# Optimization experiments

Hardware: AMD Instinct MI355X
Metric: run time of the kernel (lower is better)

The kernel has to match this reference:

```python
import jax, jax.numpy as jnp
import numpy as np

TOP_K = 2  # matches init kwarg top_k


def setup_inputs() -> dict:
    key = jax.random.key(0)
    k1, k2, k3 = jax.random.split(key, 3)
    N, D, H, E = 8192, 2048, 2048, 8
    x = jax.random.normal(k1, (N, D), dtype=jnp.float32)
    Wg = jax.random.normal(k2, (D, E), dtype=jnp.float32) * (1.0 / np.sqrt(D))
    bg = jnp.zeros((E,), dtype=jnp.float32)
    We = jax.random.normal(k3, (E, D, H), dtype=jnp.float32) * (1.0 / np.sqrt(D))
    be = jnp.zeros((E, H), dtype=jnp.float32)
    return {"x": x, "Wg": Wg, "bg": bg, "We": We, "be": be}


def reference(x, Wg, bg, We, be):
    # Gating: softmax over experts, then keep only top-k weights per token.
    gate = jax.nn.softmax(x @ Wg + bg, axis=-1)          # [N, E]
    top_v, top_i = jax.lax.top_k(gate, TOP_K)            # [N, K]
    E = gate.shape[-1]
    # Sparse combine weights: zeros except top-k entries (weights NOT renormalized,
    # matching the original which uses raw softmax scores).
    comb = jnp.sum(jax.nn.one_hot(top_i, E, dtype=gate.dtype) * top_v[..., None], axis=1)  # [N, E]
    # Per-expert linear applied to every token (dense dispatch), then weighted sum.
    expert_out = jnp.einsum('nd,edh->neh', x, We) + be   # [N, E, H]
    out = jnp.einsum('ne,neh->nh', comb, expert_out)     # [N, H]
    return out
```

## Files before the change

### kernel.cpp

```cpp
#include <hip/hip_runtime.h>

#define N_TOK 8192
#define DIM   2048
#define HID   2048
#define NE    8

typedef unsigned short u16;
typedef __attribute__((ext_vector_type(4))) float f4v;
typedef __attribute__((ext_vector_type(8))) short s8v;
typedef __attribute__((ext_vector_type(4))) unsigned short us4;
typedef __attribute__((ext_vector_type(4))) unsigned int u32x4;

__device__ __forceinline__ u16 f2bf(float f) {
  union { float f; unsigned int u; } c; c.f = f;
  unsigned int u = c.u;
  unsigned int r = (u + 0x7FFFu + ((u >> 16) & 1u)) >> 16;
  return (u16)r;
}

__device__ __forceinline__ void gll16(const void* g, void* l) {
  __builtin_amdgcn_global_load_lds(
      (const __attribute__((address_space(1))) void*)g,
      (__attribute__((address_space(3))) void*)l, 16, 0, 0);
}

__global__ __launch_bounds__(256) void gating_kernel(
    const float* __restrict__ x, const float* __restrict__ Wg,
    const float* __restrict__ bg, int* __restrict__ sel,
    float* __restrict__ wslot, u16* __restrict__ xb)
{
  __shared__ float wg_lds[NE][DIM];
  #pragma unroll
  for (int i = 0; i < 16; ++i) {
    int f = threadIdx.x + 256 * i;
    int d = f >> 1, ep = (f & 1) * 4;
    float4 w = reinterpret_cast<const float4*>(Wg)[f];
    wg_lds[ep + 0][d] = w.x; wg_lds[ep + 1][d] = w.y;
    wg_lds[ep + 2][d] = w.z; wg_lds[ep + 3][d] = w.w;
  }
  __syncthreads();

  int wave = threadIdx.x >> 6, lane = threadIdx.x & 63;
  #pragma unroll 2
  for (int j = 0; j < 4; ++j) {
    int n = blockIdx.x * 16 + wave * 4 + j;
    const float4* x4 = reinterpret_cast<const float4*>(x + (size_t)n * DIM);
    float acc[NE] = {0.f,0.f,0.f,0.f,0.f,0.f,0.f,0.f};
    #pragma unroll
    for (int i = 0; i < 8; ++i) {
      int d4 = lane + 64 * i;
      float4 xv = x4[d4];
      if (xb) {
        us4 u = {f2bf(xv.x), f2bf(xv.y), f2bf(xv.z), f2bf(xv.w)};
        *reinterpret_cast<us4*>(xb + (size_t)n * DIM + d4 * 4) = u;
      }
      #pragma unroll
      for (int e = 0; e < NE; ++e) {
        float4 w = *reinterpret_cast<const float4*>(&wg_lds[e][d4 * 4]);
        acc[e] += xv.x * w.x + xv.y * w.y + xv.z * w.z + xv.w * w.w;
      }
    }
    #pragma unroll
    for (int e = 0; e < NE; ++e)
      #pragma unroll
      for (int off = 32; off; off >>= 1)
        acc[e] += __shfl_xor(acc[e], off);

    if (lane == 0) {
      float m = -1e30f;
      #pragma unroll
      for (int e = 0; e < NE; ++e) { acc[e] += bg[e]; m = fmaxf(m, acc[e]); }
      float p[NE]; float s = 0.f;
      #pragma unroll
      for (int e = 0; e < NE; ++e) { p[e] = expf(acc[e] - m); s += p[e]; }
      float inv = 1.0f / s;
      int e1 = 0; float v1 = p[0];
      #pragma unroll
      for (int e = 1; e < NE; ++e) if (p[e] > v1) { v1 = p[e]; e1 = e; }
      int e2 = -1; float v2 = -1.f;
      #pragma unroll
      for (int e = 0; e < NE; ++e) if (e != e1 && p[e] > v2) { v2 = p[e]; e2 = e; }
      sel[n] = e1 | (e2 << 4);
      wslot[n] = v1 * inv;
      wslot[N_TOK + n] = v2 * inv;
    }
  }
}

__global__ __launch_bounds__(256) void build_lists_kernel(
    const int* __restrict__ sel, int* __restrict__ counts, int* __restrict__ lists)
{
  __shared__ int wsum[4];
  __shared__ int runbase;
  int b = blockIdx.x;
  int s = b >> 3, e = b & 7;
  int t = threadIdx.x, lane = t & 63, wave = t >> 6;
  if (t == 0) runbase = 0;
  __syncthreads();
  int* listp = lists + (size_t)b * N_TOK;
  for (int base = 0; base < N_TOK; base += 256) {
    int n = base + t;
    int sv = sel[n];
    int field = s ? (sv >> 4) : (sv & 15);
    bool p = (field == e);
    unsigned long long mask = __ballot(p);
    int rank = __popcll(mask & ((1ull << lane) - 1ull));
    int wtot = __popcll(mask);
    if (lane == 0) wsum[wave] = wtot;
    __syncthreads();
    int wbase = 0;
    #pragma unroll
    for (int w = 0; w < 4; ++w) wbase += (w < wave) ? wsum[w] : 0;
    int tot = wsum[0] + wsum[1] + wsum[2] + wsum[3];
    if (p) listp[runbase + wbase + rank] = n;
    __syncthreads();
    if (t == 0) runbase += tot;
    __syncthreads();
  }
  if (t == 0) counts[b] = runbase;
}

__global__ __launch_bounds__(256) void transpose_we_kernel(const float* __restrict__ We,
                                                           u16* __restrict__ WeT)
{
  __shared__ u16 tile[64][72];
  int e = blockIdx.z;
  int k0 = blockIdx.y * 64;
  int h0 = blockIdx.x * 64;
  const float* src = We + (size_t)e * DIM * HID + (size_t)k0 * HID + h0;
  #pragma unroll
  for (int i = 0; i < 4; ++i) {
    int flat = threadIdx.x + 256 * i;
    int kk = flat >> 4, c4 = flat & 15;
    float4 v = *reinterpret_cast<const float4*>(src + (size_t)kk * HID + c4 * 4);
    us4 u = {f2bf(v.x), f2bf(v.y), f2bf(v.z), f2bf(v.w)};
    *reinterpret_cast<us4*>(&tile[kk][c4 * 4]) = u;
  }
  __syncthreads();
  u16* dst = WeT + (size_t)e * HID * DIM + (size_t)h0 * DIM + k0;
  #pragma unroll
  for (int i = 0; i < 4; ++i) {
    int flat = threadIdx.x + 256 * i;
    int hh = flat >> 4, c4 = flat & 15;
    us4 u = {tile[c4 * 4 + 0][hh], tile[c4 * 4 + 1][hh],
             tile[c4 * 4 + 2][hh], tile[c4 * 4 + 3][hh]};
    *reinterpret_cast<us4*>(dst + (size_t)hh * DIM + c4 * 4) = u;
  }
}

__device__ __forceinline__ void mma_step(const u16* A_lds, const u16* B_lds,
                                         int lane, int wm, int wn, f4v acc[4][4])
{
  int lrow = lane & 15, lkg = lane >> 4;
  #pragma unroll
  for (int kk2 = 0; kk2 < 2; ++kk2) {
    s8v a[4], b[4];
    unsigned int koff = (unsigned int)(kk2 * 64 + lkg * 16);
    #pragma unroll
    for (int i = 0; i < 4; ++i) {
      unsigned int arow = (unsigned int)(wm + i * 16 + lrow);
      a[i] = *reinterpret_cast<const s8v*>(
          reinterpret_cast<const char*>(A_lds) + ((arow * 128u + koff) ^ ((arow & 7u) << 4)));
      unsigned int brow = (unsigned int)(wn + i * 16 + lrow);
      b[i] = *reinterpret_cast<const s8v*>(
          reinterpret_cast<const char*>(B_lds) + ((brow * 128u + koff) ^ ((brow & 7u) << 4)));
    }
    #pragma unroll
    for (int mi = 0; mi < 4; ++mi)
      #pragma unroll
      for (int ni = 0; ni < 4; ++ni)
        acc[mi][ni] = __builtin_amdgcn_mfma_f32_16x16x32_bf16(a[mi], b[ni], acc[mi][ni], 0, 0, 0);
  }
}

template <int PHASE, bool BF16SRC>
__global__ __launch_bounds__(256) void moe_gemm(
    const void* __restrict__ Asrc, const void* __restrict__ Bsrc,
    const float* __restrict__ be, const int* __restrict__ counts,
    const int* __restrict__ lists, const float* __restrict__ wslot,
    float* __restrict__ out)
{
  __shared__ __align__(16) u16 A_lds[128 * 64];
  __shared__ __align__(16) u16 B_lds[128 * 64];
  __shared__ int   tok_lds[128];
  __shared__ float wgt_lds[128];

  const int ntile = blockIdx.x;
  const int e  = blockIdx.y >> 6;
  const int mt = blockIdx.y & 63;
  const int cnt = counts[PHASE * NE + e];
  if (mt * 128 >= cnt) return;

  const int t = threadIdx.x;
  if (t < 128) {
    int r = mt * 128 + t;
    int rc = (r < cnt) ? r : (cnt - 1);
    int tok = lists[(PHASE * NE + e) * N_TOK + rc];
    tok_lds[t] = tok;
    wgt_lds[t] = wslot[PHASE * N_TOK + tok];
  }
  __syncthreads();

  const int lane = t & 63, wid = t >> 6;
  const int wm = (wid & 1) * 64, wn = (wid >> 1) * 64;

  f4v acc[4][4];
  f4v zero = {0.f, 0.f, 0.f, 0.f};
  #pragma unroll
  for (int mi = 0; mi < 4; ++mi)
    #pragma unroll
    for (int ni = 0; ni < 4; ++ni) acc[mi][ni] = zero;

  if constexpr (!BF16SRC) {
    const float* xf  = reinterpret_cast<const float*>(Asrc);
    const float* wef = reinterpret_cast<const float*>(Bsrc) + (size_t)e * DIM * HID;
    const float* ap[8]; unsigned int ab[8];
    #pragma unroll
    for (int i = 0; i < 8; ++i) {
      int flat = t + 256 * i;
      int row = flat >> 4, c4 = flat & 15;
      ap[i] = xf + (size_t)tok_lds[row] * DIM + c4 * 4;
      ab[i] = ((unsigned int)(row * 128 + c4 * 8)) ^ (((unsigned int)row & 7u) << 4);
    }
    int bn = t & 127, bh = t >> 7;
    const float* bp0 = wef + (size_t)(bh * 32) * HID + ntile * 128 + bn;
    unsigned int nswz = (((unsigned int)bn & 7u) << 4);
    for (int kt = 0; kt < DIM / 64; ++kt) {
      #pragma unroll
      for (int i = 0; i < 8; ++i) {
        float4 v = *reinterpret_cast<const float4*>(ap[i] + kt * 64);
        us4 u = {f2bf(v.x), f2bf(v.y), f2bf(v.z), f2bf(v.w)};
        *reinterpret_cast<us4*>(reinterpret_cast<char*>(A_lds) + ab[i]) = u;
      }
      const float* bp = bp0 + (size_t)(kt * 64) * HID;
      #pragma unroll
      for (int kb = 0; kb < 8; ++kb) {
        float f0 = bp[(kb * 4 + 0) * HID];
        float f1 = bp[(kb * 4 + 1) * HID];
        float f2 = bp[(kb * 4 + 2) * HID];
        float f3 = bp[(kb * 4 + 3) * HID];
        us4 u = {f2bf(f0), f2bf(f1), f2bf(f2), f2bf(f3)};
        unsigned int byte = ((unsigned int)(bn * 128 + bh * 64 + kb * 8)) ^ nswz;
        *reinterpret_cast<us4*>(reinterpret_cast<char*>(B_lds) + byte) = u;
      }
      __syncthreads();
      mma_step(A_lds, B_lds, lane, wm, wn, acc);
      __syncthreads();
    }
  } else {
    const u16* xbp = reinterpret_cast<const u16*>(Asrc);
    const u16* web = reinterpret_cast<const u16*>(Bsrc) + (size_t)e * DIM * HID;
    const int r8 = lane >> 3;
    const unsigned int ssw = ((unsigned int)((lane & 7) ^ r8)) << 4;
    const char* srcA[4]; const char* srcB[4];
    #pragma unroll
    for (int i = 0; i < 4; ++i) {
      int row = wid * 32 + i * 8 + r8;
      srcA[i] = reinterpret_cast<const char*>(xbp + (size_t)tok_lds[row] * DIM) + ssw;
      srcB[i] = reinterpret_cast<const char*>(web + (size_t)(ntile * 128 + row) * DIM) + ssw;
    }
    for (int kt = 0; kt < DIM / 64; ++kt) {
      #pragma unroll
      for (int i = 0; i < 4; ++i) {
        gll16(srcA[i] + kt * 128, reinterpret_cast<char*>(A_lds) + wid * 4096 + i * 1024);
        gll16(srcB[i] + kt * 128, reinterpret_cast<char*>(B_lds) + wid * 4096 + i * 1024);
      }
      __syncthreads();
      mma_step(A_lds, B_lds, lane, wm, wn, acc);
      __syncthreads();
    }
  }

  const float* bev = be + (size_t)e * HID + ntile * 128;
  #pragma unroll
  for (int ni = 0; ni < 4; ++ni) {
    int col = wn + ni * 16 + (lane & 15);
    float bevv = bev[col];
    #pragma unroll
    for (int mi = 0; mi < 4; ++mi) {
      #pragma unroll
      for (int q = 0; q < 4; ++q) {
        int row = wm + mi * 16 + (lane >> 4) * 4 + q;
        if (mt * 128 + row < cnt) {
          int tok = tok_lds[row];
          float w = wgt_lds[row];
          float v = w * (acc[mi][ni][q] + bevv);
          float* o = out + (size_t)tok * HID + ntile * 128 + col;
          if (PHASE == 0) *o = v; else *o += v;
        }
      }
    }
  }
}

extern "C" void kernel_launch(void* const* d_in, const int* in_sizes, int n_in,
                              void* d_out, int out_size, void* d_ws, size_t ws_size,
                              hipStream_t stream) {
  const float* x  = (const float*)d_in[0];
  const float* Wg = (const float*)d_in[1];
  const float* bg = (const float*)d_in[2];
  const float* We = (const float*)d_in[3];
  const float* be = (const float*)d_in[4];
  float* out = (float*)d_out;
  char* ws = (char*)d_ws;

  int*   counts = (int*)ws;
  int*   sel    = (int*)(ws + 256);
  float* wslot  = (float*)(ws + 256 + sizeof(int) * N_TOK);
  int*   lists  = (int*)(ws + 256 + sizeof(int) * N_TOK + sizeof(float) * 2 * N_TOK);
  size_t small_end = 256 + sizeof(int) * N_TOK + sizeof(float) * 2 * N_TOK
                   + sizeof(int) * 2 * NE * N_TOK;
  size_t off_x = (small_end + 255) & ~(size_t)255;
  size_t xbytes = (size_t)N_TOK * DIM * 2;
  size_t off_w = off_x + xbytes;
  size_t wbytes = (size_t)NE * DIM * HID * 2;
  bool full = (ws_size >= off_w + wbytes);

  u16* xb = full ? (u16*)(ws + off_x) : nullptr;

  hipLaunchKernelGGL(gating_kernel, dim3(512), dim3(256), 0, stream,
                     x, Wg, bg, sel, wslot, xb);
  hipLaunchKernelGGL(build_lists_kernel, dim3(16), dim3(256), 0, stream,
                     sel, counts, lists);

  dim3 ggrid(HID / 128, NE * (N_TOK / 128));
  if (full) {
    u16* wt = (u16*)(ws + off_w);
    hipLaunchKernelGGL(transpose_we_kernel, dim3(HID / 64, DIM / 64, NE), dim3(256), 0, stream, We, wt);
    hipLaunchKernelGGL((moe_gemm<0, true>), ggrid, dim3(256), 0, stream,
                       (const void*)xb, (const void*)wt, be, counts, lists, wslot, out);
    hipLaunchKernelGGL((moe_gemm<1, true>), ggrid, dim3(256), 0, stream,
                       (const void*)xb, (const void*)wt, be, counts, lists, wslot, out);
  } else {
    hipLaunchKernelGGL((moe_gemm<0, false>), ggrid, dim3(256), 0, stream,
                       (const void*)x, (const void*)We, be, counts, lists, wslot, out);
    hipLaunchKernelGGL((moe_gemm<1, false>), ggrid, dim3(256), 0, stream,
                       (const void*)x, (const void*)We, be, counts, lists, wslot, out);
  }
}
```

Baseline: 450.2 us.

## Compact GEMM grid with tile descriptors and chunk expert weight conversion by workspace size

A new single-thread kernel builds a compact list of (expert, row-tile) descriptors, so the grouped GEMM launches only about 71 row-tile slots instead of 512 mostly-idle blocks that exit early. The expert weight transpose/convert is also split into chunks sized to the available workspace. This allows the bf16 global_load_lds path to be used for weights even with a small workspace, at the cost of re-converting chunks between phases. With a full workspace (c=8) this runs as one transpose plus two GEMMs, so the main intended saving is fewer launched empty blocks. The serial descriptor kernel adds a small extra launch.

```diff
diff --git a/kernel.cpp b/kernel.cpp
--- a/kernel.cpp
+++ b/kernel.cpp
@@ -120,6 +120,22 @@
   if (t == 0) counts[b] = runbase;
 }
 
+__global__ void build_desc_kernel(const int* __restrict__ counts,
+                                  int* __restrict__ gfirst, int* __restrict__ desc)
+{
+  if (threadIdx.x == 0 && blockIdx.x == 0) {
+    for (int s = 0; s < 2; ++s) {
+      int tc = 0;
+      for (int e = 0; e < NE; ++e) {
+        gfirst[s * 9 + e] = tc;
+        int nt = (counts[s * NE + e] + 127) >> 7;
+        for (int i = 0; i < nt; ++i) desc[s * 71 + tc++] = (e << 8) | i;
+      }
+      gfirst[s * 9 + 8] = tc;
+    }
+  }
+}
+
 __global__ __launch_bounds__(256) void transpose_we_kernel(const float* __restrict__ We,
                                                            u16* __restrict__ WeT)
 {
@@ -173,12 +189,39 @@
   }
 }
 
-template <int PHASE, bool BF16SRC>
+__device__ __forceinline__ void gemm_epilogue(
+    const f4v acc[4][4], const float* be, const int* tok_lds, const float* wgt_lds,
+    int e, int ntile, int mt, int cnt, int lane, int wm, int wn, float* out, int phase)
+{
+  const float* bev = be + (size_t)e * HID + ntile * 128;
+  #pragma unroll
+  for (int ni = 0; ni < 4; ++ni) {
+    int col = wn + ni * 16 + (lane & 15);
+    float bevv = bev[col];
+    #pragma unroll
+    for (int mi = 0; mi < 4; ++mi) {
+      #pragma unroll
+      for (int q = 0; q < 4; ++q) {
+        int row = wm + mi * 16 + (lane >> 4) * 4 + q;
+        if (mt * 128 + row < cnt) {
+          int tok = tok_lds[row];
+          float w = wgt_lds[row];
+          float v = w * (acc[mi][ni][q] + bevv);
+          float* o = out + (size_t)tok * HID + ntile * 128 + col;
+          if (phase == 0) *o = v; else *o += v;
+        }
+      }
+    }
+  }
+}
+
+template <int PHASE, bool ABF16>
 __global__ __launch_bounds__(256) void moe_gemm(
-    const void* __restrict__ Asrc, const void* __restrict__ Bsrc,
+    const void* __restrict__ Asrc, const u16* __restrict__ wt,
     const float* __restrict__ be, const int* __restrict__ counts,
+    const int* __restrict__ gfirst, const int* __restrict__ desc,
     const int* __restrict__ lists, const float* __restrict__ wslot,
-    float* __restrict__ out)
+    float* __restrict__ out, int ce, int cnume)
 {
   __shared__ __align__(16) u16 A_lds[128 * 64];
   __shared__ __align__(16) u16 B_lds[128 * 64];
@@ -186,10 +229,14 @@
   __shared__ float wgt_lds[128];
 
   const int ntile = blockIdx.x;
-  const int e  = blockIdx.y >> 6;
-  const int mt = blockIdx.y & 63;
+  const int base = gfirst[PHASE * 9 + ce];
+  const int end  = gfirst[PHASE * 9 + ce + cnume];
+  const int idx  = base + (int)blockIdx.y;
+  if (idx >= end) return;
+  const int d  = desc[PHASE * 71 + idx];
+  const int e  = d >> 8;
+  const int mt = d & 255;
   const int cnt = counts[PHASE * NE + e];
-  if (mt * 128 >= cnt) return;
 
   const int t = threadIdx.x;
   if (t < 128) {
@@ -211,9 +258,36 @@
     #pragma unroll
     for (int ni = 0; ni < 4; ++ni) acc[mi][ni] = zero;
 
-  if constexpr (!BF16SRC) {
-    const float* xf  = reinterpret_cast<const float*>(Asrc);
-    const float* wef = reinterpret_cast<const float*>(Bsrc) + (size_t)e * DIM * HID;
+  const u16* web = wt + (size_t)(e - ce) * DIM * HID;
+  const int r8 = lane >> 3;
+  const unsigned int ssw = ((unsigned int)((lane & 7) ^ r8)) << 4;
+  const char* srcB[4];
+  #pragma unroll
+  for (int i = 0; i < 4; ++i) {
+    int row = wid * 32 + i * 8 + r8;
+    srcB[i] = reinterpret_cast<const char*>(web + (size_t)(ntile * 128 + row) * DIM) + ssw;
+  }
+
+  if constexpr (ABF16) {
+    const u16* xbp = reinterpret_cast<const u16*>(Asrc);
+    const char* srcA[4];
+    #pragma unroll
+    for (int i = 0; i < 4; ++i) {
+      int row = wid * 32 + i * 8 + r8;
+      srcA[i] = reinterpret_cast<const char*>(xbp + (size_t)tok_lds[row] * DIM) + ssw;
+    }
+    for (int kt = 0; kt < DIM / 64; ++kt) {
+      #pragma unroll
+      for (int i = 0; i < 4; ++i) {
+        gll16(srcA[i] + kt * 128, reinterpret_cast<char*>(A_lds) + wid * 4096 + i * 1024);
+        gll16(srcB[i] + kt * 128, reinterpret_cast<char*>(B_lds) + wid * 4096 + i * 1024);
+      }
+      __syncthreads();
+      mma_step(A_lds, B_lds, lane, wm, wn, acc);
+      __syncthreads();
+    }
+  } else {
+    const float* xf = reinterpret_cast<const float*>(Asrc);
     const float* ap[8]; unsigned int ab[8];
     #pragma unroll
     for (int i = 0; i < 8; ++i) {
@@ -222,75 +296,102 @@
       ap[i] = xf + (size_t)tok_lds[row] * DIM + c4 * 4;
       ab[i] = ((unsigned int)(row * 128 + c4 * 8)) ^ (((unsigned int)row & 7u) << 4);
     }
-    int bn = t & 127, bh = t >> 7;
-    const float* bp0 = wef + (size_t)(bh * 32) * HID + ntile * 128 + bn;
-    unsigned int nswz = (((unsigned int)bn & 7u) << 4);
     for (int kt = 0; kt < DIM / 64; ++kt) {
+      #pragma unroll
+      for (int i = 0; i < 4; ++i)
+        gll16(srcB[i] + kt * 128, reinterpret_cast<char*>(B_lds) + wid * 4096 + i * 1024);
       #pragma unroll
       for (int i = 0; i < 8; ++i) {
         float4 v = *reinterpret_cast<const float4*>(ap[i] + kt * 64);
         us4 u = {f2bf(v.x), f2bf(v.y), f2bf(v.z), f2bf(v.w)};
         *reinterpret_cast<us4*>(reinterpret_cast<char*>(A_lds) + ab[i]) = u;
       }
-      const float* bp = bp0 + (size_t)(kt * 64) * HID;
-      #pragma unroll
-      for (int kb = 0; kb < 8; ++kb) {
-        float f0 = bp[(kb * 4 + 0) * HID];
-        float f1 = bp[(kb * 4 + 1) * HID];
-        float f2 = bp[(kb * 4 + 2) * HID];
-        float f3 = bp[(kb * 4 + 3) * HID];
-        us4 u = {f2bf(f0), f2bf(f1), f2bf(f2), f2bf(f3)};
-        unsigned int byte = ((unsigned int)(bn * 128 + bh * 64 + kb * 8)) ^ nswz;
-        *reinterpret_cast<us4*>(reinterpret_cast<char*>(B_lds) + byte) = u;
-      }
       __syncthreads();
       mma_step(A_lds, B_lds, lane, wm, wn, acc);
       __syncthreads();
     }
-  } else {
-    const u16* xbp = reinterpret_cast<const u16*>(Asrc);
-    const u16* web = reinterpret_cast<const u16*>(Bsrc) + (size_t)e * DIM * HID;
-    const int r8 = lane >> 3;
-    const unsigned int ssw = ((unsigned int)((lane & 7) ^ r8)) << 4;
-    const char* srcA[4]; const char* srcB[4];
-    #pragma unroll
-    for (int i = 0; i < 4; ++i) {
-      int row = wid * 32 + i * 8 + r8;
-      srcA[i] = reinterpret_cast<const char*>(xbp + (size_t)tok_lds[row] * DIM) + ssw;
-      srcB[i] = reinterpret_cast<const char*>(web + (size_t)(ntile * 128 + row) * DIM) + ssw;
-    }
-    for (int kt = 0; kt < DIM / 64; ++kt) {
-      #pragma unroll
-      for (int i = 0; i < 4; ++i) {
-        gll16(srcA[i] + kt * 128, reinterpret_cast<char*>(A_lds) + wid * 4096 + i * 1024);
-        gll16(srcB[i] + kt * 128, reinterpret_cast<char*>(B_lds) + wid * 4096 + i * 1024);
-      }
-      __syncthreads();
-      mma_step(A_lds, B_lds, lane, wm, wn, acc);
-      __syncthreads();
-    }
-  }
-
-  const float* bev = be + (size_t)e * HID + ntile * 128;
-  #pragma unroll
-  for (int ni = 0; ni < 4; ++ni) {
-    int col = wn + ni * 16 + (lane & 15);
-    float bevv = bev[col];
-    #pragma unroll
-    for (int mi = 0; mi < 4; ++mi) {
-      #pragma unroll
-      for (int q = 0; q < 4; ++q) {
-        int row = wm + mi * 16 + (lane >> 4) * 4 + q;
-        if (mt * 128 + row < cnt) {
-          int tok = tok_lds[row];
-          float w = wgt_lds[row];
-          float v = w * (acc[mi][ni][q] + bevv);
-          float* o = out + (size_t)tok * HID + ntile * 128 + col;
-          if (PHASE == 0) *o = v; else *o += v;
-        }
-      }
-    }
-  }
+  }
+
+  gemm_epilogue(acc, be, tok_lds, wgt_lds, e, ntile, mt, cnt, lane, wm, wn, out, PHASE);
+}
+
+template <int PHASE>
+__global__ __launch_bounds__(256) void moe_gemm_f32b(
+    const float* __restrict__ xf, const float* __restrict__ Wef,
+    const float* __restrict__ be, const int* __restrict__ counts,
+    const int* __restrict__ gfirst, const int* __restrict__ desc,
+    const int* __restrict__ lists, const float* __restrict__ wslot,
+    float* __restrict__ out)
+{
+  __shared__ __align__(16) u16 A_lds[128 * 64];
+  __shared__ __align__(16) u16 B_lds[128 * 64];
+  __shared__ int   tok_lds[128];
+  __shared__ float wgt_lds[128];
+
+  const int ntile = blockIdx.x;
+  const int idx = gfirst[PHASE * 9 + 0] + (int)blockIdx.y;
+  if (idx >= gfirst[PHASE * 9 + 8]) return;
+  const int d  = desc[PHASE * 71 + idx];
+  const int e  = d >> 8;
+  const int mt = d & 255;
+  const int cnt = counts[PHASE * NE + e];
+
+  const int t = threadIdx.x;
+  if (t < 128) {
+    int r = mt * 128 + t;
+    int rc = (r < cnt) ? r : (cnt - 1);
+    int tok = lists[(PHASE * NE + e) * N_TOK + rc];
+    tok_lds[t] = tok;
+    wgt_lds[t] = wslot[PHASE * N_TOK + tok];
+  }
+  __syncthreads();
+
+  const int lane = t & 63, wid = t >> 6;
+  const int wm = (wid & 1) * 64, wn = (wid >> 1) * 64;
+
+  f4v acc[4][4];
+  f4v zero = {0.f, 0.f, 0.f, 0.f};
+  #pragma unroll
+  for (int mi = 0; mi < 4; ++mi)
+    #pragma unroll
+    for (int ni = 0; ni < 4; ++ni) acc[mi][ni] = zero;
+
+  const float* wef = Wef + (size_t)e * DIM * HID;
+  const float* ap[8]; unsigned int ab[8];
+  #pragma unroll
+  for (int i = 0; i < 8; ++i) {
+    int flat = t + 256 * i;
+    int row = flat >> 4, c4 = flat & 15;
+    ap[i] = xf + (size_t)tok_lds[row] * DIM + c4 * 4;
+    ab[i] = ((unsigned int)(row * 128 + c4 * 8)) ^ (((unsigned int)row & 7u) << 4);
+  }
+  int bn = t & 127, bh = t >> 7;
+  const float* bp0 = wef + (size_t)(bh * 32) * HID + ntile * 128 + bn;
+  unsigned int nswz = (((unsigned int)bn & 7u) << 4);
+  for (int kt = 0; kt < DIM / 64; ++kt) {
+    #pragma unroll
+    for (int i = 0; i < 8; ++i) {
+      float4 v = *reinterpret_cast<const float4*>(ap[i] + kt * 64);
+      us4 u = {f2bf(v.x), f2bf(v.y), f2bf(v.z), f2bf(v.w)};
+      *reinterpret_cast<us4*>(reinterpret_cast<char*>(A_lds) + ab[i]) = u;
+    }
+    const float* bp = bp0 + (size_t)(kt * 64) * HID;
+    #pragma unroll
+    for (int kb = 0; kb < 8; ++kb) {
+      float f0 = bp[(kb * 4 + 0) * HID];
+      float f1 = bp[(kb * 4 + 1) * HID];
+      float f2 = bp[(kb * 4 + 2) * HID];
+      float f3 = bp[(kb * 4 + 3) * HID];
+      us4 u = {f2bf(f0), f2bf(f1), f2bf(f2), f2bf(f3)};
+      unsigned int byte = ((unsigned int)(bn * 128 + bh * 64 + kb * 8)) ^ nswz;
+      *reinterpret_cast<us4*>(reinterpret_cast<char*>(B_lds) + byte) = u;
+    }
+    __syncthreads();
+    mma_step(A_lds, B_lds, lane, wm, wn, acc);
+    __syncthreads();
+  }
+
+  gemm_epilogue(acc, be, tok_lds, wgt_lds, e, ntile, mt, cnt, lane, wm, wn, out, PHASE);
 }
 
 extern "C" void kernel_launch(void* const* d_in, const int* in_sizes, int n_in,
@@ -305,36 +406,55 @@
   char* ws = (char*)d_ws;
 
   int*   counts = (int*)ws;
-  int*   sel    = (int*)(ws + 256);
-  float* wslot  = (float*)(ws + 256 + sizeof(int) * N_TOK);
-  int*   lists  = (int*)(ws + 256 + sizeof(int) * N_TOK + sizeof(float) * 2 * N_TOK);
-  size_t small_end = 256 + sizeof(int) * N_TOK + sizeof(float) * 2 * N_TOK
-                   + sizeof(int) * 2 * NE * N_TOK;
-  size_t off_x = (small_end + 255) & ~(size_t)255;
-  size_t xbytes = (size_t)N_TOK * DIM * 2;
-  size_t off_w = off_x + xbytes;
-  size_t wbytes = (size_t)NE * DIM * HID * 2;
-  bool full = (ws_size >= off_w + wbytes);
-
-  u16* xb = full ? (u16*)(ws + off_x) : nullptr;
+  int*   gfirst = (int*)(ws + 64);
+  int*   desc   = (int*)(ws + 256);
+  int*   sel    = (int*)(ws + 1024);
+  float* wslot  = (float*)(ws + 33792);
+  int*   lists  = (int*)(ws + 99328);
+  const size_t base_end = 623616;
+  const size_t xbsz = (size_t)N_TOK * DIM * 2;
+  const size_t pe   = (size_t)DIM * HID * 2;
+
+  int c = 0; bool use_xb = false;
+  const int cands[4] = {8, 4, 2, 1};
+  for (int i = 0; i < 4; ++i) {
+    int cc = cands[i];
+    if (base_end + xbsz + (size_t)cc * pe <= ws_size) { c = cc; use_xb = true; break; }
+    if (base_end + (size_t)cc * pe <= ws_size)        { c = cc; use_xb = false; break; }
+  }
+  u16* xb = use_xb ? (u16*)(ws + base_end) : nullptr;
+  u16* wt = (c > 0) ? (u16*)(ws + base_end + (use_xb ? xbsz : 0)) : nullptr;
 
   hipLaunchKernelGGL(gating_kernel, dim3(512), dim3(256), 0, stream,
                      x, Wg, bg, sel, wslot, xb);
   hipLaunchKernelGGL(build_lists_kernel, dim3(16), dim3(256), 0, stream,
                      sel, counts, lists);
-
-  dim3 ggrid(HID / 128, NE * (N_TOK / 128));
-  if (full) {
-    u16* wt = (u16*)(ws + off_w);
-    hipLaunchKernelGGL(transpose_we_kernel, dim3(HID / 64, DIM / 64, NE), dim3(256), 0, stream, We, wt);
-    hipLaunchKernelGGL((moe_gemm<0, true>), ggrid, dim3(256), 0, stream,
-                       (const void*)xb, (const void*)wt, be, counts, lists, wslot, out);
-    hipLaunchKernelGGL((moe_gemm<1, true>), ggrid, dim3(256), 0, stream,
-                       (const void*)xb, (const void*)wt, be, counts, lists, wslot, out);
+  hipLaunchKernelGGL(build_desc_kernel, dim3(1), dim3(64), 0, stream,
+                     counts, gfirst, desc);
+
+  if (c > 0) {
+    const int nc = NE / c;
+    dim3 tgrid(HID / 64, DIM / 64, c);
+    dim3 ggrid(HID / 128, 63 + c);
+    #define LAUNCH_T(ch) hipLaunchKernelGGL(transpose_we_kernel, tgrid, dim3(256), 0, stream, \
+                           We + (size_t)(ch) * c * DIM * HID, wt)
+    #define LAUNCH_G(PH, ch) do { \
+        if (use_xb) hipLaunchKernelGGL((moe_gemm<PH, true>), ggrid, dim3(256), 0, stream, \
+            (const void*)xb, wt, be, counts, gfirst, desc, lists, wslot, out, (ch) * c, c); \
+        else        hipLaunchKernelGGL((moe_gemm<PH, false>), ggrid, dim3(256), 0, stream, \
+            (const void*)x,  wt, be, counts, gfirst, desc, lists, wslot, out, (ch) * c, c); \
+      } while (0)
+
+    for (int i = 0; i < nc; ++i) { LAUNCH_T(i); LAUNCH_G(0, i); }
+    LAUNCH_G(1, nc - 1);
+    for (int i = nc - 2; i >= 0; --i) { LAUNCH_T(i); LAUNCH_G(1, i); }
+    #undef LAUNCH_T
+    #undef LAUNCH_G
   } else {
-    hipLaunchKernelGGL((moe_gemm<0, false>), ggrid, dim3(256), 0, stream,
-                       (const void*)x, (const void*)We, be, counts, lists, wslot, out);
-    hipLaunchKernelGGL((moe_gemm<1, false>), ggrid, dim3(256), 0, stream,
-                       (const void*)x, (const void*)We, be, counts, lists, wslot, out);
-  }
-}
+    dim3 ggrid(HID / 128, 71);
+    hipLaunchKernelGGL((moe_gemm_f32b<0>), ggrid, dim3(256), 0, stream,
+                       x, We, be, counts, gfirst, desc, lists, wslot, out);
+    hipLaunchKernelGGL((moe_gemm_f32b<1>), ggrid, dim3(256), 0, stream,
+                       x, We, be, counts, gfirst, desc, lists, wslot, out);
+  }
+}
```

New measurement: 451.6 us. About the same (+0.3%).

## Drop bf16 pre-conversion, fuse fp32 conversion into GEMM with register prefetch and compact tile grid

Applied to the files above, without the earlier changes.

Removes the separate We transpose/convert kernel and the bf16 copy of x. The MoE GEMM now reads fp32 inputs directly and converts them to bf16 in registers. The next K-tile is prefetched into registers while the current one runs on MFMA. A descriptor kernel builds a compact list of non-empty (expert, m-tile) pairs, launched over a swizzled 1D grid so blocks no longer exit early. In exchange, the strided scalar fp32 loads of We for the B operand stay uncoalesced and are repeated for every m-tile, and register pressure rises from the 32+ prefetch registers.

```diff
diff --git a/kernel.cpp b/kernel.cpp
--- a/kernel.cpp
+++ b/kernel.cpp
@@ -4,12 +4,12 @@
 #define DIM   2048
 #define HID   2048
 #define NE    8
+#define NKT   (DIM / 64)
 
 typedef unsigned short u16;
 typedef __attribute__((ext_vector_type(4))) float f4v;
 typedef __attribute__((ext_vector_type(8))) short s8v;
 typedef __attribute__((ext_vector_type(4))) unsigned short us4;
-typedef __attribute__((ext_vector_type(4))) unsigned int u32x4;
 
 __device__ __forceinline__ u16 f2bf(float f) {
   union { float f; unsigned int u; } c; c.f = f;
@@ -18,16 +18,10 @@
   return (u16)r;
 }
 
-__device__ __forceinline__ void gll16(const void* g, void* l) {
-  __builtin_amdgcn_global_load_lds(
-      (const __attribute__((address_space(1))) void*)g,
-      (__attribute__((address_space(3))) void*)l, 16, 0, 0);
-}
-
 __global__ __launch_bounds__(256) void gating_kernel(
     const float* __restrict__ x, const float* __restrict__ Wg,
     const float* __restrict__ bg, int* __restrict__ sel,
-    float* __restrict__ wslot, u16* __restrict__ xb)
+    float* __restrict__ wslot)
 {
   __shared__ float wg_lds[NE][DIM];
   #pragma unroll
@@ -50,10 +44,6 @@
     for (int i = 0; i < 8; ++i) {
       int d4 = lane + 64 * i;
       float4 xv = x4[d4];
-      if (xb) {
-        us4 u = {f2bf(xv.x), f2bf(xv.y), f2bf(xv.z), f2bf(xv.w)};
-        *reinterpret_cast<us4*>(xb + (size_t)n * DIM + d4 * 4) = u;
-      }
       #pragma unroll
       for (int e = 0; e < NE; ++e) {
         float4 w = *reinterpret_cast<const float4*>(&wg_lds[e][d4 * 4]);
@@ -120,31 +110,19 @@
   if (t == 0) counts[b] = runbase;
 }
 
-__global__ __launch_bounds__(256) void transpose_we_kernel(const float* __restrict__ We,
-                                                           u16* __restrict__ WeT)
-{
-  __shared__ u16 tile[64][72];
-  int e = blockIdx.z;
-  int k0 = blockIdx.y * 64;
-  int h0 = blockIdx.x * 64;
-  const float* src = We + (size_t)e * DIM * HID + (size_t)k0 * HID + h0;
-  #pragma unroll
-  for (int i = 0; i < 4; ++i) {
-    int flat = threadIdx.x + 256 * i;
-    int kk = flat >> 4, c4 = flat & 15;
-    float4 v = *reinterpret_cast<const float4*>(src + (size_t)kk * HID + c4 * 4);
-    us4 u = {f2bf(v.x), f2bf(v.y), f2bf(v.z), f2bf(v.w)};
-    *reinterpret_cast<us4*>(&tile[kk][c4 * 4]) = u;
-  }
-  __syncthreads();
-  u16* dst = WeT + (size_t)e * HID * DIM + (size_t)h0 * DIM + k0;
-  #pragma unroll
-  for (int i = 0; i < 4; ++i) {
-    int flat = threadIdx.x + 256 * i;
-    int hh = flat >> 4, c4 = flat & 15;
-    us4 u = {tile[c4 * 4 + 0][hh], tile[c4 * 4 + 1][hh],
-             tile[c4 * 4 + 2][hh], tile[c4 * 4 + 3][hh]};
-    *reinterpret_cast<us4*>(dst + (size_t)hh * DIM + c4 * 4) = u;
+__global__ void build_desc_kernel(const int* __restrict__ counts,
+                                  int* __restrict__ gfirst, int* __restrict__ desc)
+{
+  if (threadIdx.x == 0 && blockIdx.x == 0) {
+    for (int s = 0; s < 2; ++s) {
+      int tc = 0;
+      for (int e = 0; e < NE; ++e) {
+        gfirst[s * 9 + e] = tc;
+        int nt = (counts[s * NE + e] + 127) >> 7;
+        for (int i = 0; i < nt; ++i) desc[s * 71 + tc++] = (e << 8) | i;
+      }
+      gfirst[s * 9 + 8] = tc;
+    }
   }
 }
 
@@ -173,10 +151,11 @@
   }
 }
 
-template <int PHASE, bool BF16SRC>
-__global__ __launch_bounds__(256) void moe_gemm(
-    const void* __restrict__ Asrc, const void* __restrict__ Bsrc,
+template <int PHASE>
+__global__ __launch_bounds__(256) void moe_gemm_f32(
+    const float* __restrict__ xf, const float* __restrict__ Wef,
     const float* __restrict__ be, const int* __restrict__ counts,
+    const int* __restrict__ gfirst, const int* __restrict__ desc,
     const int* __restrict__ lists, const float* __restrict__ wslot,
     float* __restrict__ out)
 {
@@ -185,11 +164,15 @@
   __shared__ int   tok_lds[128];
   __shared__ float wgt_lds[128];
 
-  const int ntile = blockIdx.x;
-  const int e  = blockIdx.y >> 6;
-  const int mt = blockIdx.y & 63;
+  const int lin = blockIdx.x;
+  const int swz = (lin & 7) * 142 + (lin >> 3);
+  const int ntile = swz / 71;
+  const int idx   = swz % 71;
+  if (idx >= gfirst[PHASE * 9 + 8]) return;
+  const int d  = desc[PHASE * 71 + idx];
+  const int e  = d >> 8;
+  const int mt = d & 255;
   const int cnt = counts[PHASE * NE + e];
-  if (mt * 128 >= cnt) return;
 
   const int t = threadIdx.x;
   if (t < 128) {
@@ -211,65 +194,62 @@
     #pragma unroll
     for (int ni = 0; ni < 4; ++ni) acc[mi][ni] = zero;
 
-  if constexpr (!BF16SRC) {
-    const float* xf  = reinterpret_cast<const float*>(Asrc);
-    const float* wef = reinterpret_cast<const float*>(Bsrc) + (size_t)e * DIM * HID;
-    const float* ap[8]; unsigned int ab[8];
-    #pragma unroll
-    for (int i = 0; i < 8; ++i) {
-      int flat = t + 256 * i;
-      int row = flat >> 4, c4 = flat & 15;
-      ap[i] = xf + (size_t)tok_lds[row] * DIM + c4 * 4;
-      ab[i] = ((unsigned int)(row * 128 + c4 * 8)) ^ (((unsigned int)row & 7u) << 4);
-    }
-    int bn = t & 127, bh = t >> 7;
-    const float* bp0 = wef + (size_t)(bh * 32) * HID + ntile * 128 + bn;
-    unsigned int nswz = (((unsigned int)bn & 7u) << 4);
-    for (int kt = 0; kt < DIM / 64; ++kt) {
-      #pragma unroll
-      for (int i = 0; i < 8; ++i) {
-        float4 v = *reinterpret_cast<const float4*>(ap[i] + kt * 64);
-        us4 u = {f2bf(v.x), f2bf(v.y), f2bf(v.z), f2bf(v.w)};
-        *reinterpret_cast<us4*>(reinterpret_cast<char*>(A_lds) + ab[i]) = u;
-      }
-      const float* bp = bp0 + (size_t)(kt * 64) * HID;
-      #pragma unroll
-      for (int kb = 0; kb < 8; ++kb) {
-        float f0 = bp[(kb * 4 + 0) * HID];
-        float f1 = bp[(kb * 4 + 1) * HID];
-        float f2 = bp[(kb * 4 + 2) * HID];
-        float f3 = bp[(kb * 4 + 3) * HID];
-        us4 u = {f2bf(f0), f2bf(f1), f2bf(f2), f2bf(f3)};
-        unsigned int byte = ((unsigned int)(bn * 128 + bh * 64 + kb * 8)) ^ nswz;
-        *reinterpret_cast<us4*>(reinterpret_cast<char*>(B_lds) + byte) = u;
-      }
-      __syncthreads();
-      mma_step(A_lds, B_lds, lane, wm, wn, acc);
-      __syncthreads();
-    }
-  } else {
-    const u16* xbp = reinterpret_cast<const u16*>(Asrc);
-    const u16* web = reinterpret_cast<const u16*>(Bsrc) + (size_t)e * DIM * HID;
-    const int r8 = lane >> 3;
-    const unsigned int ssw = ((unsigned int)((lane & 7) ^ r8)) << 4;
-    const char* srcA[4]; const char* srcB[4];
-    #pragma unroll
-    for (int i = 0; i < 4; ++i) {
-      int row = wid * 32 + i * 8 + r8;
-      srcA[i] = reinterpret_cast<const char*>(xbp + (size_t)tok_lds[row] * DIM) + ssw;
-      srcB[i] = reinterpret_cast<const char*>(web + (size_t)(ntile * 128 + row) * DIM) + ssw;
-    }
-    for (int kt = 0; kt < DIM / 64; ++kt) {
-      #pragma unroll
-      for (int i = 0; i < 4; ++i) {
-        gll16(srcA[i] + kt * 128, reinterpret_cast<char*>(A_lds) + wid * 4096 + i * 1024);
-        gll16(srcB[i] + kt * 128, reinterpret_cast<char*>(B_lds) + wid * 4096 + i * 1024);
-      }
-      __syncthreads();
-      mma_step(A_lds, B_lds, lane, wm, wn, acc);
-      __syncthreads();
-    }
-  }
+  const float* wef = Wef + (size_t)e * DIM * HID;
+  const float* ap[8]; unsigned int ab[8];
+  #pragma unroll
+  for (int i = 0; i < 8; ++i) {
+    int flat = t + 256 * i;
+    int row = flat >> 4, c4 = flat & 15;
+    ap[i] = xf + (size_t)tok_lds[row] * DIM + c4 * 4;
+    ab[i] = ((unsigned int)(row * 128 + c4 * 8)) ^ (((unsigned int)row & 7u) << 4);
+  }
+  const int bn = t & 127, bh = t >> 7;
+  const float* bp0 = wef + (size_t)(bh * 32) * HID + ntile * 128 + bn;
+  const unsigned int nswz = (((unsigned int)bn & 7u) << 4);
+
+  float4 av[8];
+  float  bv[32];
+
+#define LOAD_STAGE(KT) do {                                                     \
+    _Pragma("unroll") for (int i = 0; i < 8; ++i)                               \
+      av[i] = *reinterpret_cast<const float4*>(ap[i] + (KT) * 64);              \
+    const float* bpk = bp0 + (size_t)(KT) * 64 * HID;                           \
+    _Pragma("unroll") for (int kb = 0; kb < 8; ++kb) {                          \
+      _Pragma("unroll") for (int r = 0; r < 4; ++r)                             \
+        bv[kb * 4 + r] = bpk[(size_t)(kb * 4 + r) * HID];                       \
+    }                                                                           \
+  } while (0)
+
+#define WRITE_STAGE() do {                                                      \
+    _Pragma("unroll") for (int i = 0; i < 8; ++i) {                             \
+      us4 u = {f2bf(av[i].x), f2bf(av[i].y), f2bf(av[i].z), f2bf(av[i].w)};     \
+      *reinterpret_cast<us4*>(reinterpret_cast<char*>(A_lds) + ab[i]) = u;      \
+    }                                                                           \
+    _Pragma("unroll") for (int kb = 0; kb < 8; ++kb) {                          \
+      us4 u = {f2bf(bv[kb*4+0]), f2bf(bv[kb*4+1]),                              \
+               f2bf(bv[kb*4+2]), f2bf(bv[kb*4+3])};                             \
+      unsigned int byte = ((unsigned int)(bn * 128 + bh * 64 + kb * 8)) ^ nswz; \
+      *reinterpret_cast<us4*>(reinterpret_cast<char*>(B_lds) + byte) = u;       \
+    }                                                                           \
+  } while (0)
+
+  LOAD_STAGE(0);
+  WRITE_STAGE();
+  __syncthreads();
+
+  #pragma unroll 1
+  for (int kt = 0; kt < NKT - 1; ++kt) {
+    LOAD_STAGE(kt + 1);
+    asm volatile("" ::: "memory");
+    mma_step(A_lds, B_lds, lane, wm, wn, acc);
+    __syncthreads();
+    WRITE_STAGE();
+    __syncthreads();
+  }
+  mma_step(A_lds, B_lds, lane, wm, wn, acc);
+
+#undef LOAD_STAGE
+#undef WRITE_STAGE
 
   const float* bev = be + (size_t)e * HID + ntile * 128;
   #pragma unroll
@@ -305,36 +285,22 @@
   char* ws = (char*)d_ws;
 
   int*   counts = (int*)ws;
-  int*   sel    = (int*)(ws + 256);
-  float* wslot  = (float*)(ws + 256 + sizeof(int) * N_TOK);
-  int*   lists  = (int*)(ws + 256 + sizeof(int) * N_TOK + sizeof(float) * 2 * N_TOK);
-  size_t small_end = 256 + sizeof(int) * N_TOK + sizeof(float) * 2 * N_TOK
-                   + sizeof(int) * 2 * NE * N_TOK;
-  size_t off_x = (small_end + 255) & ~(size_t)255;
-  size_t xbytes = (size_t)N_TOK * DIM * 2;
-  size_t off_w = off_x + xbytes;
-  size_t wbytes = (size_t)NE * DIM * HID * 2;
-  bool full = (ws_size >= off_w + wbytes);
-
-  u16* xb = full ? (u16*)(ws + off_x) : nullptr;
+  int*   gfirst = (int*)(ws + 64);
+  int*   desc   = (int*)(ws + 256);
+  int*   sel    = (int*)(ws + 1024);
+  float* wslot  = (float*)(ws + 33792);
+  int*   lists  = (int*)(ws + 99328);
 
   hipLaunchKernelGGL(gating_kernel, dim3(512), dim3(256), 0, stream,
-                     x, Wg, bg, sel, wslot, xb);
+                     x, Wg, bg, sel, wslot);
   hipLaunchKernelGGL(build_lists_kernel, dim3(16), dim3(256), 0, stream,
                      sel, counts, lists);
-
-  dim3 ggrid(HID / 128, NE * (N_TOK / 128));
-  if (full) {
-    u16* wt = (u16*)(ws + off_w);
-    hipLaunchKernelGGL(transpose_we_kernel, dim3(HID / 64, DIM / 64, NE), dim3(256), 0, stream, We, wt);
-    hipLaunchKernelGGL((moe_gemm<0, true>), ggrid, dim3(256), 0, stream,
-                       (const void*)xb, (const void*)wt, be, counts, lists, wslot, out);
-    hipLaunchKernelGGL((moe_gemm<1, true>), ggrid, dim3(256), 0, stream,
-                       (const void*)xb, (const void*)wt, be, counts, lists, wslot, out);
-  } else {
-    hipLaunchKernelGGL((moe_gemm<0, false>), ggrid, dim3(256), 0, stream,
-                       (const void*)x, (const void*)We, be, counts, lists, wslot, out);
-    hipLaunchKernelGGL((moe_gemm<1, false>), ggrid, dim3(256), 0, stream,
-                       (const void*)x, (const void*)We, be, counts, lists, wslot, out);
-  }
-}
+  hipLaunchKernelGGL(build_desc_kernel, dim3(1), dim3(64), 0, stream,
+                     counts, gfirst, desc);
+
+  dim3 ggrid(16 * 71);
+  hipLaunchKernelGGL((moe_gemm_f32<0>), ggrid, dim3(256), 0, stream,
+                     x, We, be, counts, gfirst, desc, lists, wslot, out);
+  hipLaunchKernelGGL((moe_gemm_f32<1>), ggrid, dim3(256), 0, stream,
+                     x, We, be, counts, gfirst, desc, lists, wslot, out);
+}
```

Measured after the change: 830.3 us. +84.4%, slower.
